# Kernel tuning notes

Measured on AMD Instinct MI355X. Metric: run time of the kernel, lower is better.

Reference implementation:

```python
import jax, jax.numpy as jnp
import numpy as np

# Model dims (per init_kwargs)
DIM = 512
HEADS = 8
HD = DIM // HEADS          # head_dim = 64
NA = 32                    # num_agent_tokens
B, N = 4, 16384            # batch, flattened super-token count
SCALE = HD ** -0.5
NEG = -1e9                 # masked-softmax fill


def setup_inputs() -> dict:
    key = jax.random.key(0)
    ks = jax.random.split(key, 7)
    x = jax.random.normal(ks[0], (B, N, DIM), jnp.float32)
    mask = jax.random.randint(ks[1], (B, N), 0, 2).astype(jnp.int32)  # per-sample token validity mask
    agent_tokens = jax.random.normal(ks[2], (NA, DIM), jnp.float32) * 0.02  # trunc_normal(std=0.02) analog
    Wq = jax.random.normal(ks[3], (DIM, DIM), jnp.float32) / np.sqrt(DIM)
    Wk = jax.random.normal(ks[4], (DIM, DIM), jnp.float32) / np.sqrt(DIM)
    Wv = jax.random.normal(ks[5], (DIM, DIM), jnp.float32) / np.sqrt(DIM)
    Wproj = jax.random.normal(ks[6], (DIM, DIM), jnp.float32) / np.sqrt(DIM)
    return {"x": x, "mask": mask, "agent_tokens": agent_tokens,
            "Wq": Wq, "Wk": Wk, "Wv": Wv, "Wproj": Wproj}


def reference(x, mask, agent_tokens, Wq, Wk, Wv, Wproj):
    Bv, Nv, C = x.shape

    def heads(t):  # [B, N, C] -> [B, H, N, hd]
        return t.reshape(Bv, -1, HEADS, HD).transpose(0, 2, 1, 3)

    q = heads(x @ Wq)
    k = heads(x @ Wk)
    v = heads(x @ Wv)
    # agents: [Na, C] -> [B, H, Na, hd] (shared across batch)
    a = jnp.broadcast_to(
        agent_tokens.reshape(1, NA, HEADS, HD).transpose(0, 2, 1, 3),
        (Bv, HEADS, NA, HD))

    key_mask = (mask > 0)[:, None, None, :]              # [B,1,1,N]

    # Stage 1: agents attend to (masked) keys
    agent_attn = jnp.einsum('bhad,bhkd->bhak', a, k) * SCALE
    agent_attn = jnp.where(key_mask, agent_attn, NEG)
    agent_attn = jax.nn.softmax(agent_attn, axis=-1)
    agent_v = jnp.einsum('bhak,bhkd->bhad', agent_attn, v)  # [B,H,Na,hd]

    # Stage 2: queries attend to agents
    q_attn = jax.nn.softmax(jnp.einsum('bhqd,bhad->bhqa', q, a) * SCALE, axis=-1)
    out = jnp.einsum('bhqa,bhad->bhqd', q_attn, agent_v)     # [B,H,N,hd]

    out = out.transpose(0, 2, 1, 3).reshape(Bv, Nv, C) @ Wproj
    out = out * (mask > 0)[:, :, None].astype(out.dtype)    # zero invalid tokens
    return out
```

## Files before the change

### kernel.cpp

```cpp
#include <hip/hip_runtime.h>


typedef float  f32x4   __attribute__((ext_vector_type(4)));
typedef short  bf16x8  __attribute__((ext_vector_type(8)));
typedef unsigned short u16x4 __attribute__((ext_vector_type(4)));
typedef unsigned short u16x8 __attribute__((ext_vector_type(8)));

#define MFMA16(a, b, c) __builtin_amdgcn_mfma_f32_16x16x32_bf16((a), (b), (c), 0, 0, 0)

__device__ __forceinline__ unsigned short f2bf(float f) {
    unsigned u = __builtin_bit_cast(unsigned, f);
    u += 0x7FFFu + ((u >> 16) & 1u);
    return (unsigned short)(u >> 16);
}
__device__ __forceinline__ void gl2lds16(const void* g, void* l) {
    __builtin_amdgcn_global_load_lds(
        (const __attribute__((address_space(1))) unsigned int*)g,
        (__attribute__((address_space(3))) unsigned int*)l, 16, 0, 0);
}

__global__ __launch_bounds__(256) void k_cvt_x(const float* __restrict__ x,
                                               unsigned char* __restrict__ xt) {
    int v = blockIdx.x * 256 + threadIdx.x;
    int tile = v >> 10;
    int q = v & 1023;
    int row = q >> 3, c = q & 7;
    int mt = tile >> 3, ks = tile & 7;
    const float* sp = x + ((size_t)(mt * 128 + row)) * 512 + ks * 64 + c * 8;
    float4 v0 = *(const float4*)sp;
    float4 v1 = *(const float4*)(sp + 4);
    u16x8 o;
    o[0] = f2bf(v0.x); o[1] = f2bf(v0.y); o[2] = f2bf(v0.z); o[3] = f2bf(v0.w);
    o[4] = f2bf(v1.x); o[5] = f2bf(v1.y); o[6] = f2bf(v1.z); o[7] = f2bf(v1.w);
    *(u16x8*)(xt + (size_t)tile * 16384 + row * 128 + ((c ^ (row & 7)) << 4)) = o;
}

__global__ __launch_bounds__(256) void k_w_t_p(const float* __restrict__ Wp,
                                               unsigned short* __restrict__ Wpt) {
    __shared__ float t[32][33];
    const int k0 = blockIdx.y * 32, n0 = blockIdx.x * 32;
#pragma unroll
    for (int j = 0; j < 4; ++j) {
        int i = threadIdx.x + 256 * j;
        int ky = i >> 5, nx = i & 31;
        t[ky][nx] = Wp[(size_t)(k0 + ky) * 512 + n0 + nx];
    }
    __syncthreads();
#pragma unroll
    for (int j = 0; j < 4; ++j) {
        int i = threadIdx.x + 256 * j;
        int ny = i >> 5, kx = i & 31;
        Wpt[(size_t)(n0 + ny) * 512 + k0 + kx] = f2bf(t[kx][ny]);
    }
}

__global__ __launch_bounds__(256) void k_w_tile(const float* __restrict__ Wv,
                                                unsigned char* __restrict__ wtl2) {
    const int ks = blockIdx.x, nt = blockIdx.y;
    unsigned char* dst = wtl2 + ((size_t)(nt * 8 + ks)) * 16384;
    const int row = threadIdx.x & 63;
#pragma unroll
    for (int cc = 0; cc < 2; ++cc) {
        int c = (threadIdx.x >> 6) + cc * 4;
        u16x8 o;
#pragma unroll
        for (int j = 0; j < 8; ++j)
            o[j] = f2bf(Wv[(size_t)(ks * 64 + c * 8 + j) * 512 + nt * 64 + row]);
        *(u16x8*)(dst + row * 128 + ((c ^ (row & 7)) << 4)) = o;
    }
}

__global__ __launch_bounds__(256) void k_akw(const float* __restrict__ at,
                                             const float* __restrict__ Wk,
                                             const float* __restrict__ Wq,
                                             unsigned char* __restrict__ wtl2) {
    const int ks = blockIdx.x, h = blockIdx.y, which = blockIdx.z;
    const float* W = which ? Wq : Wk;
    const int row = threadIdx.x >> 3, c8 = threadIdx.x & 7;
    const float* ar = at + row * 512 + h * 64;
    float accv[8];
#pragma unroll
    for (int j = 0; j < 8; ++j) {
        const float* wr = W + (size_t)(ks * 64 + c8 * 8 + j) * 512 + h * 64;
        float s = 0.f;
#pragma unroll 8
        for (int d = 0; d < 64; ++d) s += ar[d] * wr[d];
        accv[j] = s;
    }
    u16x8 o;
#pragma unroll
    for (int j = 0; j < 8; ++j) o[j] = f2bf(accv[j]);
    *(u16x8*)(wtl2 + ((size_t)(h * 8 + ks)) * 16384 + 8192 + which * 4096 +
              row * 128 + ((c8 ^ (row & 7)) << 4)) = o;
}

__global__ __launch_bounds__(256) void k_qkvs(const unsigned char* __restrict__ xt,
                                              const unsigned char* __restrict__ wtl2,
                                              const int* __restrict__ mask,
                                              unsigned char* __restrict__ Qat,
                                              float* __restrict__ part_pv,
                                              float* __restrict__ part_ml) {
    __shared__ __align__(16) unsigned char S_[32768];
    unsigned char* As = S_;
    unsigned char* Bs = S_ + 16384;
    const int tid = threadIdx.x, l = tid & 63, wid = tid >> 6;
    const int g = l >> 4, lr = l & 15;
    const int wm = wid >> 1, wn = wid & 1;
    const int dd = blockIdx.x;
    const int nt = (dd >> 3) & 7;
    const int mt = (dd & 7) + ((dd >> 6) << 3);
    const int m0 = mt * 128;
    const int b = mt >> 7, chunk = mt & 127, bh = b * 8 + nt;

    f32x4 acc[4][4] = {};

    for (int ks = 0; ks < 8; ++ks) {
        const size_t abase = ((size_t)(mt * 8 + ks)) * 16384;
        const size_t bbase = ((size_t)(nt * 8 + ks)) * 16384;
#pragma unroll
        for (int i = 0; i < 4; ++i)
            gl2lds16(xt + abase + i * 4096 + tid * 16, As + i * 4096 + tid * 16);
#pragma unroll
        for (int i = 0; i < 4; ++i)
            gl2lds16(wtl2 + bbase + i * 4096 + tid * 16, Bs + i * 4096 + tid * 16);
        __syncthreads();

        bf16x8 af[4][2];
#pragma unroll
        for (int mf = 0; mf < 4; ++mf) {
            int row = wm * 64 + mf * 16 + lr;
#pragma unroll
            for (int k2 = 0; k2 < 2; ++k2)
                af[mf][k2] = *(const bf16x8*)(As + row * 128 + (((k2 * 4 + g) ^ (row & 7)) << 4));
        }
#pragma unroll
        for (int k2 = 0; k2 < 2; ++k2) {
#pragma unroll
            for (int nf = 0; nf < 4; ++nf) {
                const int regio = wn ? (8192 + (nf >> 1) * 4096) : 0;
                const int brow = (wn ? ((nf & 1) * 16) : (nf * 16)) + lr;
                bf16x8 bv = *(const bf16x8*)(Bs + regio + brow * 128 +
                                             (((k2 * 4 + g) ^ (brow & 7)) << 4));
#pragma unroll
                for (int mf = 0; mf < 4; ++mf)
                    acc[mf][nf] = MFMA16(af[mf][k2], bv, acc[mf][nf]);
            }
        }
        __syncthreads();
    }

    unsigned char* Ph0 = S_;
    unsigned char* Evh = S_ + 9216;
    float* redM = (float*)(S_ + 27648);
    float* redL = (float*)(S_ + 27904);
    float* avsH = (float*)S_;

    float sc2[4][2][4];
    float Mb[2];

    if (wn == 0) {
        unsigned char* Ev = Evh + wm * 9216;
#pragma unroll
        for (int mf = 0; mf < 4; ++mf)
#pragma unroll
            for (int vf = 0; vf < 4; ++vf) {
                int d5 = vf * 16 + lr;
                u16x4 vv;
                vv[0] = f2bf(acc[mf][vf][0]); vv[1] = f2bf(acc[mf][vf][1]);
                vv[2] = f2bf(acc[mf][vf][2]); vv[3] = f2bf(acc[mf][vf][3]);
                *(u16x4*)(Ev + d5 * 144 + mf * 32 + g * 8) = vv;
            }
    } else {
        const size_t qbase = ((size_t)(mt * 4 + (nt >> 1))) * 16384;
        const int c80 = (nt & 1) * 4 + (lr >> 3);
#pragma unroll
        for (int mf = 0; mf < 4; ++mf) {
#pragma unroll
            for (int r = 0; r < 4; ++r) {
                float v0 = acc[mf][2][r] * 0.125f, v1 = acc[mf][3][r] * 0.125f;
                float m = fmaxf(v0, v1);
                m = fmaxf(m, __shfl_xor(m, 1));
                m = fmaxf(m, __shfl_xor(m, 2));
                m = fmaxf(m, __shfl_xor(m, 4));
                m = fmaxf(m, __shfl_xor(m, 8));
                float e0 = __expf(v0 - m), e1 = __expf(v1 - m);
                float s = e0 + e1;
                s += __shfl_xor(s, 1);
                s += __shfl_xor(s, 2);
                s += __shfl_xor(s, 4);
                s += __shfl_xor(s, 8);
                float inv = 1.0f / s;
                int row = wm * 64 + mf * 16 + g * 4 + r;
                size_t rb = qbase + row * 128 + (lr & 7) * 2;
                *(unsigned short*)(Qat + rb + ((c80 ^ (row & 7)) << 4)) = f2bf(e0 * inv);
                *(unsigned short*)(Qat + rb + (((c80 + 2) ^ (row & 7)) << 4)) = f2bf(e1 * inv);
            }
        }
#pragma unroll
        for (int mf = 0; mf < 4; ++mf) {
            int4 mv = *(const int4*)(mask + m0 + wm * 64 + mf * 16 + g * 4);
            int mvr[4] = {mv.x, mv.y, mv.z, mv.w};
#pragma unroll
            for (int sf = 0; sf < 2; ++sf)
#pragma unroll
                for (int r = 0; r < 4; ++r)
                    sc2[mf][sf][r] = (mvr[r] > 0) ? acc[mf][sf][r] * 0.125f : -1.0e9f;
        }
#pragma unroll
        for (int sf = 0; sf < 2; ++sf) {
            float m = sc2[0][sf][0];
#pragma unroll
            for (int mf = 0; mf < 4; ++mf)
#pragma unroll
                for (int r = 0; r < 4; ++r) m = fmaxf(m, sc2[mf][sf][r]);
            m = fmaxf(m, __shfl_xor(m, 16));
            m = fmaxf(m, __shfl_xor(m, 32));
            if (g == 0) redM[wm * 32 + sf * 16 + lr] = m;
        }
    }
    __syncthreads();

    if (wn == 1) {
        float le[2] = {0.f, 0.f};
#pragma unroll
        for (int sf = 0; sf < 2; ++sf) {
            int ag = sf * 16 + lr;
            Mb[sf] = fmaxf(redM[ag], redM[32 + ag]);
        }
        unsigned char* Ph = Ph0 + wm * 4608;
#pragma unroll
        for (int mf = 0; mf < 4; ++mf)
#pragma unroll
            for (int sf = 0; sf < 2; ++sf) {
                u16x4 p4;
#pragma unroll
                for (int r = 0; r < 4; ++r) {
                    float p = __expf(sc2[mf][sf][r] - Mb[sf]);
                    le[sf] += p;
                    p4[r] = f2bf(p);
                }
                int ag = sf * 16 + lr;
                *(u16x4*)(Ph + ag * 144 + mf * 32 + g * 8) = p4;
            }
#pragma unroll
        for (int sf = 0; sf < 2; ++sf) {
            le[sf] += __shfl_xor(le[sf], 16);
            le[sf] += __shfl_xor(le[sf], 32);
            if (g == 0) redL[wm * 32 + sf * 16 + lr] = le[sf];
        }
    }
    __syncthreads();

    const unsigned char* Ph = Ph0 + wm * 4608;
    const unsigned char* Ev = Evh + wm * 9216;
    bf16x8 pa[2];
#pragma unroll
    for (int agf = 0; agf < 2; ++agf) {
        int ag = agf * 16 + lr;
        pa[agf] = *(const bf16x8*)(Ph + ag * 144 + wn * 64 + g * 16);
    }
    f32x4 pv[2][4] = {};
#pragma unroll
    for (int vf = 0; vf < 4; ++vf) {
        int d5 = vf * 16 + lr;
        bf16x8 bv = *(const bf16x8*)(Ev + d5 * 144 + wn * 64 + g * 16);
#pragma unroll
        for (int agf = 0; agf < 2; ++agf)
            pv[agf][vf] = MFMA16(pa[agf], bv, pv[agf][vf]);
    }
    __syncthreads();

    float* pout = part_pv + ((size_t)bh * 128 + chunk) * 2048;
#pragma unroll
    for (int agf = 0; agf < 2; ++agf) {
#pragma unroll
        for (int vf = 0; vf < 4; ++vf)
#pragma unroll
            for (int r = 0; r < 4; ++r)
                avsH[wid * 1024 + (g * 4 + r) * 64 + vf * 16 + lr] = pv[agf][vf][r];
        __syncthreads();
#pragma unroll
        for (int j = 0; j < 4; ++j) {
            int idx = tid + 256 * j;
            pout[agf * 1024 + idx] = avsH[idx] + avsH[1024 + idx] +
                                     avsH[2048 + idx] + avsH[3072 + idx];
        }
        if (agf == 0) __syncthreads();
    }
    if (wid == 1 && g == 0) {
        size_t o = ((size_t)bh * 128 + chunk) * 64;
        float L0 = redL[lr] + redL[32 + lr];
        float L1 = redL[16 + lr] + redL[48 + lr];
        part_ml[o + lr * 2] = Mb[0];
        part_ml[o + lr * 2 + 1] = L0;
        part_ml[o + (16 + lr) * 2] = Mb[1];
        part_ml[o + (16 + lr) * 2 + 1] = L1;
    }
}

__global__ __launch_bounds__(256) void k_agent_comb(const float* __restrict__ part_pv,
                                                    const float* __restrict__ part_ml,
                                                    unsigned short* __restrict__ avbf) {
    __shared__ float scl[128][4];
    __shared__ float iLg[4], Mg[4];
    const int tid = threadIdx.x;
    const int ag0 = blockIdx.x * 4, bh = blockIdx.y;
    if (tid < 4) {
        int ag = ag0 + tid;
        const float* ml = part_ml + (size_t)bh * 8192 + ag * 2;
        float M = -3.0e38f;
#pragma unroll 4
        for (int c = 0; c < 128; ++c) M = fmaxf(M, ml[c * 64]);
        float L = 0.f;
#pragma unroll 4
        for (int c = 0; c < 128; ++c) L += __expf(ml[c * 64] - M) * ml[c * 64 + 1];
        Mg[tid] = M; iLg[tid] = 1.0f / L;
    }
    __syncthreads();
#pragma unroll
    for (int it = 0; it < 2; ++it) {
        int idx = tid + 256 * it;
        int c = idx >> 2, agl = idx & 3;
        scl[c][agl] = __expf(part_ml[(size_t)bh * 8192 + (size_t)c * 64 + (ag0 + agl) * 2] - Mg[agl]);
    }
    __syncthreads();
    const int agl = tid >> 6, d5 = tid & 63;
    const float* pv = part_pv + (size_t)bh * 128 * 2048 + (size_t)(ag0 + agl) * 64 + d5;
    float a = 0.f;
#pragma unroll 4
    for (int c = 0; c < 128; ++c) a += scl[c][agl] * pv[(size_t)c * 2048];
    avbf[(size_t)bh * 2048 + (size_t)(ag0 + agl) * 64 + d5] = f2bf(a * iLg[agl]);
}

__global__ __launch_bounds__(64) void k_avp(const unsigned short* __restrict__ avbf,
                                            const unsigned short* __restrict__ Wpt,
                                            unsigned char* __restrict__ AVPt) {
    const int l = threadIdx.x & 63;
    const int bh = blockIdx.x, b = bh >> 3, h = bh & 7;
    const int g = l >> 4, lr = l & 15;
    bf16x8 avf[2][2];
#pragma unroll
    for (int mf = 0; mf < 2; ++mf)
#pragma unroll
        for (int ks = 0; ks < 2; ++ks)
            avf[mf][ks] = *(const bf16x8*)(avbf + (size_t)bh * 2048 + (mf * 16 + lr) * 64 + ks * 32 + g * 8);
    const int kst = h >> 1;
#pragma unroll 4
    for (int nf = 0; nf < 32; ++nf) {
        int j = nf * 16 + lr;
        bf16x8 w0 = *(const bf16x8*)(Wpt + (size_t)j * 512 + h * 64 + g * 8);
        bf16x8 w1 = *(const bf16x8*)(Wpt + (size_t)j * 512 + h * 64 + 32 + g * 8);
        int jt = j >> 7, row = j & 127;
#pragma unroll
        for (int mf = 0; mf < 2; ++mf) {
            f32x4 z = {0.f, 0.f, 0.f, 0.f};
            f32x4 acc = MFMA16(avf[mf][0], w0, z);
            acc = MFMA16(avf[mf][1], w1, acc);
            u16x4 o;
            o[0] = f2bf(acc[0]); o[1] = f2bf(acc[1]); o[2] = f2bf(acc[2]); o[3] = f2bf(acc[3]);
            int c8 = (h & 1) * 4 + mf * 2 + (g >> 1);
            size_t byte = ((size_t)((b * 4 + jt) * 4 + kst)) * 16384 + row * 128 +
                          ((c8 ^ (row & 7)) << 4) + (g & 1) * 8;
            *(u16x4*)(AVPt + byte) = o;
        }
    }
}

__global__ __launch_bounds__(256) void k_out(const unsigned char* __restrict__ Qat,
                                             const unsigned char* __restrict__ AVPt,
                                             const int* __restrict__ mask,
                                             float* __restrict__ out) {
    __shared__ __align__(16) unsigned char As[16384];
    __shared__ __align__(16) unsigned char Bs[16384];
    const int tid = threadIdx.x, l = tid & 63, wid = tid >> 6;
    const int wm = wid >> 1, wn = wid & 1;
    const int g = l >> 4, lr = l & 15;
    const int d = blockIdx.x;
    const int nt = (d >> 3) & 3;
    const int mt = (d & 7) + ((d >> 5) << 3);
    const int m0 = mt * 128, j0 = nt * 128;
    const int b = m0 >> 14;
    f32x4 acc[4][4] = {};

    for (int ks = 0; ks < 4; ++ks) {
        const size_t abase = ((size_t)(mt * 4 + ks)) * 16384;
        const size_t bbase = ((size_t)((b * 4 + nt) * 4 + ks)) * 16384;
#pragma unroll
        for (int i = 0; i < 4; ++i) {
            gl2lds16(Qat + abase + i * 4096 + tid * 16, As + i * 4096 + tid * 16);
            gl2lds16(AVPt + bbase + i * 4096 + tid * 16, Bs + i * 4096 + tid * 16);
        }
        __syncthreads();
        bf16x8 af[4][2];
#pragma unroll
        for (int mf = 0; mf < 4; ++mf) {
            int row = wm * 64 + mf * 16 + lr;
#pragma unroll
            for (int k2 = 0; k2 < 2; ++k2)
                af[mf][k2] = *(const bf16x8*)(As + row * 128 + (((k2 * 4 + g) ^ (row & 7)) << 4));
        }
#pragma unroll
        for (int k2 = 0; k2 < 2; ++k2) {
#pragma unroll
            for (int nf = 0; nf < 4; ++nf) {
                int brow = wn * 64 + nf * 16 + lr;
                bf16x8 bv = *(const bf16x8*)(Bs + brow * 128 + (((k2 * 4 + g) ^ (brow & 7)) << 4));
#pragma unroll
                for (int mf = 0; mf < 4; ++mf)
                    acc[mf][nf] = MFMA16(af[mf][k2], bv, acc[mf][nf]);
            }
        }
        __syncthreads();
    }
#pragma unroll
    for (int mf = 0; mf < 4; ++mf) {
        int trow = m0 + wm * 64 + mf * 16 + g * 4;
#pragma unroll
        for (int r = 0; r < 4; ++r) {
            float mv = (mask[trow + r] > 0) ? 1.0f : 0.0f;
#pragma unroll
            for (int nf = 0; nf < 4; ++nf) {
                int j = j0 + wn * 64 + nf * 16 + lr;
                out[(size_t)(trow + r) * 512 + j] = acc[mf][nf][r] * mv;
            }
        }
    }
}

extern "C" void kernel_launch(void* const* d_in, const int* in_sizes, int n_in,
                              void* d_out, int out_size, void* d_ws, size_t ws_size,
                              hipStream_t stream) {
    const float* x  = (const float*)d_in[0];
    const int*  mk  = (const int*)d_in[1];
    const float* at = (const float*)d_in[2];
    const float* Wq = (const float*)d_in[3];
    const float* Wk = (const float*)d_in[4];
    const float* Wv = (const float*)d_in[5];
    const float* Wp = (const float*)d_in[6];
    float* out = (float*)d_out;
    char* ws = (char*)d_ws;

    unsigned char*  xt    = (unsigned char*)(ws);
    float* part_pv = (float*)(ws + ((size_t)64 << 20));
    float* part_ml = (float*)(ws + ((size_t)100 << 20));
    unsigned char*  Qat   = (unsigned char*)(ws + ((size_t)192 << 20));
    unsigned short* Wpt   = (unsigned short*)(ws + ((size_t)256 << 20));
    unsigned char*  wtl2  = (unsigned char*)(ws + ((size_t)258 << 20));
    unsigned short* avbf  = (unsigned short*)(ws + ((size_t)259 << 20) + (576 << 10));
    unsigned char*  AVPt  = (unsigned char*)(ws + ((size_t)260 << 20));

    k_cvt_x<<<16384, 256, 0, stream>>>(x, xt);
    k_w_t_p<<<dim3(16, 16), 256, 0, stream>>>(Wp, Wpt);
    k_w_tile<<<dim3(8, 8), 256, 0, stream>>>(Wv, wtl2);
    k_akw<<<dim3(8, 8, 2), 256, 0, stream>>>(at, Wk, Wq, wtl2);
    k_qkvs<<<4096, 256, 0, stream>>>(xt, wtl2, mk, Qat, part_pv, part_ml);
    k_agent_comb<<<dim3(8, 32), 256, 0, stream>>>(part_pv, part_ml, avbf);
    k_avp<<<32, 64, 0, stream>>>(avbf, Wpt, AVPt);
    k_out<<<2048, 256, 0, stream>>>(Qat, AVPt, mk, out);
}
```

Measured before the change: 241.5 us.

## Fuse fp32-to-bf16 conversion of x into QKV GEMM and split k_avp grid

Drops the separate k_cvt_x pass, which wrote a bf16 swizzled copy of x. The GEMM now DMAs fp32 x tiles straight into LDS with an XOR swizzle and converts them to bf16 in registers using v_cvt_pk_bf16_f32 before the MFMAs. This removes one full read-write round trip of x and one launch, but doubles the A-tile LDS footprint (48KB total), which may cut occupancy, and re-reads fp32 x for each of the 8 column tiles. Separately, k_avp is split across 4x more blocks to parallelize a tiny kernel.

```diff
diff --git a/kernel.cpp b/kernel.cpp
--- a/kernel.cpp
+++ b/kernel.cpp
@@ -3,6 +3,7 @@
 
 typedef float  f32x4   __attribute__((ext_vector_type(4)));
 typedef short  bf16x8  __attribute__((ext_vector_type(8)));
+typedef unsigned int   u32x4 __attribute__((ext_vector_type(4)));
 typedef unsigned short u16x4 __attribute__((ext_vector_type(4)));
 typedef unsigned short u16x8 __attribute__((ext_vector_type(8)));
 
@@ -13,26 +14,15 @@
     u += 0x7FFFu + ((u >> 16) & 1u);
     return (unsigned short)(u >> 16);
 }
+__device__ __forceinline__ unsigned cvtpk_bf16(float lo, float hi) {
+    unsigned r;
+    asm("v_cvt_pk_bf16_f32 %0, %1, %2" : "=v"(r) : "v"(lo), "v"(hi));
+    return r;
+}
 __device__ __forceinline__ void gl2lds16(const void* g, void* l) {
     __builtin_amdgcn_global_load_lds(
         (const __attribute__((address_space(1))) unsigned int*)g,
         (__attribute__((address_space(3))) unsigned int*)l, 16, 0, 0);
-}
-
-__global__ __launch_bounds__(256) void k_cvt_x(const float* __restrict__ x,
-                                               unsigned char* __restrict__ xt) {
-    int v = blockIdx.x * 256 + threadIdx.x;
-    int tile = v >> 10;
-    int q = v & 1023;
-    int row = q >> 3, c = q & 7;
-    int mt = tile >> 3, ks = tile & 7;
-    const float* sp = x + ((size_t)(mt * 128 + row)) * 512 + ks * 64 + c * 8;
-    float4 v0 = *(const float4*)sp;
-    float4 v1 = *(const float4*)(sp + 4);
-    u16x8 o;
-    o[0] = f2bf(v0.x); o[1] = f2bf(v0.y); o[2] = f2bf(v0.z); o[3] = f2bf(v0.w);
-    o[4] = f2bf(v1.x); o[5] = f2bf(v1.y); o[6] = f2bf(v1.z); o[7] = f2bf(v1.w);
-    *(u16x8*)(xt + (size_t)tile * 16384 + row * 128 + ((c ^ (row & 7)) << 4)) = o;
 }
 
 __global__ __launch_bounds__(256) void k_w_t_p(const float* __restrict__ Wp,
@@ -94,15 +84,15 @@
               row * 128 + ((c8 ^ (row & 7)) << 4)) = o;
 }
 
-__global__ __launch_bounds__(256) void k_qkvs(const unsigned char* __restrict__ xt,
+__global__ __launch_bounds__(256) void k_qkvs(const float* __restrict__ x,
                                               const unsigned char* __restrict__ wtl2,
                                               const int* __restrict__ mask,
                                               unsigned char* __restrict__ Qat,
                                               float* __restrict__ part_pv,
                                               float* __restrict__ part_ml) {
-    __shared__ __align__(16) unsigned char S_[32768];
+    __shared__ __align__(16) unsigned char S_[49152];
     unsigned char* As = S_;
-    unsigned char* Bs = S_ + 16384;
+    unsigned char* Bs = S_ + 32768;
     const int tid = threadIdx.x, l = tid & 63, wid = tid >> 6;
     const int g = l >> 4, lr = l & 15;
     const int wm = wid >> 1, wn = wid & 1;
@@ -112,14 +102,18 @@
     const int m0 = mt * 128;
     const int b = mt >> 7, chunk = mt & 127, bh = b * 8 + nt;
 
+    const int arow0 = tid >> 4;
+    const int ac = (tid & 15) ^ arow0;
+    const float* asrc = x + (size_t)(m0 + arow0) * 512 + ac * 4;
+
     f32x4 acc[4][4] = {};
 
     for (int ks = 0; ks < 8; ++ks) {
-        const size_t abase = ((size_t)(mt * 8 + ks)) * 16384;
+        const float* ap = asrc + ks * 64;
+#pragma unroll
+        for (int i = 0; i < 8; ++i)
+            gl2lds16(ap + (size_t)i * 8192, As + i * 4096 + tid * 16);
         const size_t bbase = ((size_t)(nt * 8 + ks)) * 16384;
-#pragma unroll
-        for (int i = 0; i < 4; ++i)
-            gl2lds16(xt + abase + i * 4096 + tid * 16, As + i * 4096 + tid * 16);
 #pragma unroll
         for (int i = 0; i < 4; ++i)
             gl2lds16(wtl2 + bbase + i * 4096 + tid * 16, Bs + i * 4096 + tid * 16);
@@ -128,10 +122,19 @@
         bf16x8 af[4][2];
 #pragma unroll
         for (int mf = 0; mf < 4; ++mf) {
-            int row = wm * 64 + mf * 16 + lr;
-#pragma unroll
-            for (int k2 = 0; k2 < 2; ++k2)
-                af[mf][k2] = *(const bf16x8*)(As + row * 128 + (((k2 * 4 + g) ^ (row & 7)) << 4));
+            const int rowb = (wm * 64 + mf * 16 + lr) * 256;
+#pragma unroll
+            for (int k2 = 0; k2 < 2; ++k2) {
+                const int s0 = k2 * 8 + g * 2;
+                f32x4 p0 = *(const f32x4*)(As + rowb + ((s0 ^ lr) << 4));
+                f32x4 p1 = *(const f32x4*)(As + rowb + (((s0 + 1) ^ lr) << 4));
+                u32x4 w;
+                w[0] = cvtpk_bf16(p0[0], p0[1]);
+                w[1] = cvtpk_bf16(p0[2], p0[3]);
+                w[2] = cvtpk_bf16(p1[0], p1[1]);
+                w[3] = cvtpk_bf16(p1[2], p1[3]);
+                af[mf][k2] = __builtin_bit_cast(bf16x8, w);
+            }
         }
 #pragma unroll
         for (int k2 = 0; k2 < 2; ++k2) {
@@ -336,7 +339,7 @@
                                             const unsigned short* __restrict__ Wpt,
                                             unsigned char* __restrict__ AVPt) {
     const int l = threadIdx.x & 63;
-    const int bh = blockIdx.x, b = bh >> 3, h = bh & 7;
+    const int q = blockIdx.x, bh = blockIdx.y, b = bh >> 3, h = bh & 7;
     const int g = l >> 4, lr = l & 15;
     bf16x8 avf[2][2];
 #pragma unroll
@@ -345,8 +348,8 @@
         for (int ks = 0; ks < 2; ++ks)
             avf[mf][ks] = *(const bf16x8*)(avbf + (size_t)bh * 2048 + (mf * 16 + lr) * 64 + ks * 32 + g * 8);
     const int kst = h >> 1;
-#pragma unroll 4
-    for (int nf = 0; nf < 32; ++nf) {
+#pragma unroll
+    for (int nf = q * 8; nf < q * 8 + 8; ++nf) {
         int j = nf * 16 + lr;
         bf16x8 w0 = *(const bf16x8*)(Wpt + (size_t)j * 512 + h * 64 + g * 8);
         bf16x8 w1 = *(const bf16x8*)(Wpt + (size_t)j * 512 + h * 64 + 32 + g * 8);
@@ -440,7 +443,6 @@
     float* out = (float*)d_out;
     char* ws = (char*)d_ws;
 
-    unsigned char*  xt    = (unsigned char*)(ws);
     float* part_pv = (float*)(ws + ((size_t)64 << 20));
     float* part_ml = (float*)(ws + ((size_t)100 << 20));
     unsigned char*  Qat   = (unsigned char*)(ws + ((size_t)192 << 20));
@@ -449,12 +451,11 @@
     unsigned short* avbf  = (unsigned short*)(ws + ((size_t)259 << 20) + (576 << 10));
     unsigned char*  AVPt  = (unsigned char*)(ws + ((size_t)260 << 20));
 
-    k_cvt_x<<<16384, 256, 0, stream>>>(x, xt);
     k_w_t_p<<<dim3(16, 16), 256, 0, stream>>>(Wp, Wpt);
     k_w_tile<<<dim3(8, 8), 256, 0, stream>>>(Wv, wtl2);
     k_akw<<<dim3(8, 8, 2), 256, 0, stream>>>(at, Wk, Wq, wtl2);
-    k_qkvs<<<4096, 256, 0, stream>>>(xt, wtl2, mk, Qat, part_pv, part_ml);
+    k_qkvs<<<4096, 256, 0, stream>>>(x, wtl2, mk, Qat, part_pv, part_ml);
     k_agent_comb<<<dim3(8, 32), 256, 0, stream>>>(part_pv, part_ml, avbf);
-    k_avp<<<32, 64, 0, stream>>>(avbf, Wpt, AVPt);
+    k_avp<<<dim3(4, 32), 64, 0, stream>>>(avbf, Wpt, AVPt);
     k_out<<<2048, 256, 0, stream>>>(Qat, AVPt, mk, out);
 }
```

After: 289.7 us. 20.0% more time.
